# Performance work log

Hardware: AMD Instinct MI355X
Metric: run time of the kernel (lower is better)

## Reference

```python
import jax, jax.numpy as jnp
import numpy as np

N, K = 4096, 12          # nodes, incoming edges per node
E = N * K                # bonds
INPUT_DIM = 128
N_HEADS = 16
HEAD_DIM = 8
OUT_DIM = N_HEADS * HEAD_DIM   # 128
NUM_GAUSS = 20
NUM_ANG_FUNCS = 3              # AngularEncoding -> 1 + 3*2*2 = 13 dims
A_DIM = 1 + NUM_ANG_FUNCS * 4
KV_DIM = INPUT_DIM + 2 * NUM_GAUSS + A_DIM  # 181
Q_DIM = INPUT_DIM


def _build_graph_and_triplets():
    # edge e = i*K + t-1 : row=(i+t)%N -> col=i  (K incoming edges per node)
    col = np.repeat(np.arange(N), K)
    row = (col + np.tile(np.arange(1, K + 1), N)) % N
    bond_index = np.stack([row, col]).astype(np.int64)  # [2, E]
    # triplets: for edge e=(j->i), pair with every incoming edge (k->j) of j
    idx_ji = np.repeat(np.arange(E), K)
    idx_kj = np.repeat(row, K) * K + np.tile(np.arange(K), E)
    idx_i = col[idx_ji]
    idx_j = row[idx_ji]
    idx_k = row[idx_kj]
    mask = idx_i != idx_k
    return (bond_index, idx_i[mask], idx_j[mask], idx_k[mask],
            idx_kj[mask], idx_ji[mask])


def setup_inputs() -> dict:
    key = jax.random.key(0)
    ks = jax.random.split(key, 8)
    bond_index, idx_i, idx_j, idx_k, idx_kj, idx_ji = _build_graph_and_triplets()
    w = 0.05
    return {
        "h": jax.random.normal(ks[0], (N, INPUT_DIM), dtype=jnp.float32),
        "h_bond": jax.random.normal(ks[1], (E, INPUT_DIM), dtype=jnp.float32),
        "pos": jax.random.normal(ks[2], (N, 3), dtype=jnp.float32),
        "bond_index": jnp.asarray(bond_index),
        "idx_i": jnp.asarray(idx_i), "idx_j": jnp.asarray(idx_j),
        "idx_k": jnp.asarray(idx_k), "idx_kj": jnp.asarray(idx_kj),
        "idx_ji": jnp.asarray(idx_ji),
        "W_key": jax.random.normal(ks[3], (KV_DIM, OUT_DIM), dtype=jnp.float32) * w,
        "W_value": jax.random.normal(ks[4], (KV_DIM, OUT_DIM), dtype=jnp.float32) * w,
        "W_query": jax.random.normal(ks[5], (Q_DIM, OUT_DIM), dtype=jnp.float32) * w,
        "W_edge0": jax.random.normal(ks[6], (NUM_GAUSS, OUT_DIM), dtype=jnp.float32) * w,
        "W_edge1": jax.random.normal(ks[7], (NUM_GAUSS, OUT_DIM), dtype=jnp.float32) * w,
    }


def reference(h, h_bond, pos, bond_index, idx_i, idx_j, idx_k, idx_kj, idx_ji,
              W_key, W_value, W_query, W_edge0, W_edge1):
    Eb = h_bond.shape[0]
    row, col = bond_index[0], bond_index[1]
    # per-bond distance + Gaussian smearing (start=0, stop=10, 20 gaussians)
    dist = jnp.sqrt(jnp.sum((pos[col] - pos[row]) ** 2, axis=-1))  # [E]
    offset = jnp.linspace(0.0, 10.0, NUM_GAUSS)
    coeff = -0.5 / (offset[1] - offset[0]) ** 2
    r_feat = jnp.exp(coeff * (dist[:, None] - offset) ** 2)        # [E, 20]
    # per-triplet angle + angular encoding
    pos_i = pos[idx_i]
    pos_ji = pos[idx_j] - pos_i
    pos_ki = pos[idx_k] - pos_i
    a = jnp.sum(pos_ji * pos_ki, axis=-1)
    b = jnp.linalg.norm(jnp.cross(pos_ji, pos_ki), axis=-1)
    angle = jnp.arctan2(b, a)                                      # [T]
    t = jnp.arange(1, NUM_ANG_FUNCS + 1, dtype=jnp.float32)
    freq = jnp.concatenate([t, 1.0 / t])                           # [6]
    x = angle[:, None]
    a_feat = jnp.concatenate([x, jnp.sin(x * freq), jnp.cos(x * freq)], axis=-1)  # [T,13]
    # triplet gathers
    r_kj, r_ji = r_feat[idx_kj], r_feat[idx_ji]
    kv_input = jnp.concatenate([h_bond[idx_kj], r_kj, r_ji, a_feat], axis=-1)  # [T,181]
    q_input = h_bond[idx_ji]                                                    # [T,128]
    T = kv_input.shape[0]
    k_proj = (kv_input @ W_key).reshape(T, N_HEADS, HEAD_DIM)
    v_proj = (kv_input @ W_value).reshape(T, N_HEADS, HEAD_DIM)
    q_proj = (q_input @ W_query).reshape(T, N_HEADS, HEAD_DIM)
    edge_attn = jnp.tanh(r_ji @ W_edge0).reshape(T, N_HEADS, HEAD_DIM)
    alpha = jnp.sum(q_proj * k_proj * edge_attn, axis=-1) / np.sqrt(HEAD_DIM)   # [T,H]
    # segment softmax over idx_ji (torch_geometric softmax semantics)
    m = jax.lax.stop_gradient(jax.ops.segment_max(alpha, idx_ji, num_segments=Eb))
    ex = jnp.exp(alpha - m[idx_ji])
    s = jax.ops.segment_sum(ex, idx_ji, num_segments=Eb)
    alpha = ex / (s[idx_ji] + 1e-16)
    msg = v_proj * jnp.tanh(r_ji @ W_edge1).reshape(T, N_HEADS, HEAD_DIM)
    msg = msg * alpha[:, :, None]
    out = jax.ops.segment_sum(msg, idx_ji, num_segments=Eb)  # [E,H,D]
    return out.reshape(Eb, OUT_DIM)
```

## Files before the change

### kernel.cpp

```cpp
#include <hip/hip_runtime.h>
#include <math.h>

#define INPUT_DIM 128
#define OUT_DIM 128
#define NUM_GAUSS 20
#define NH 16
#define BM 64
#define MAXT 16
#define WPB 4
#define SCALE 0.35355339059327373f


static __device__ __forceinline__ void wave_lds_fence() {
    __asm__ volatile("s_waitcnt lgkmcnt(0)" ::: "memory");
    __builtin_amdgcn_wave_barrier();
}

__global__ __launch_bounds__(256, 3) void bond_proj_kernel(
    const float* __restrict__ h_bond,
    const float* __restrict__ pos,
    const int*   __restrict__ bond_index,
    const float* __restrict__ Wk,
    const float* __restrict__ Wv,
    const float* __restrict__ Wq,
    const float* __restrict__ We0,
    float* __restrict__ r_out,
    float* __restrict__ KB,
    float* __restrict__ VB,
    float* __restrict__ QE,
    int E)
{
    __shared__ float As[BM * 148];
    const int tid = threadIdx.x;
    const int e0 = blockIdx.x * BM;

    for (int i = tid; i < BM * 32; i += 256) {
        int e = i >> 5, c = (i & 31) << 2;
        float4 v = make_float4(0.f, 0.f, 0.f, 0.f);
        if (e0 + e < E) v = *(const float4*)&h_bond[(size_t)(e0 + e) * INPUT_DIM + c];
        float* dst = &As[e * 148 + c];
        dst[0] = v.x; dst[1] = v.y; dst[2] = v.z; dst[3] = v.w;
    }
    {
        const float step = 10.f / (NUM_GAUSS - 1);
        const float coeff = -0.5f / (step * step);
        for (int i = tid; i < BM * NUM_GAUSS; i += 256) {
            int e = i / NUM_GAUSS, g = i % NUM_GAUSS;
            int ge = e0 + e;
            float rv = 0.f;
            if (ge < E) {
                int jrow = bond_index[ge];
                int icol = bond_index[E + ge];
                float dx = pos[icol*3+0] - pos[jrow*3+0];
                float dy = pos[icol*3+1] - pos[jrow*3+1];
                float dz = pos[icol*3+2] - pos[jrow*3+2];
                float dist = sqrtf(dx*dx + dy*dy + dz*dz);
                float t = dist - g * step;
                rv = __expf(coeff * t * t);
                r_out[(size_t)ge * NUM_GAUSS + g] = rv;
            }
            As[e * 148 + 128 + g] = rv;
        }
    }
    __syncthreads();

    const int em = tid >> 5;
    const int dn = (tid & 31) << 2;
    const float* AsB = &As[em * 8 * 148];

    float aK[8][4], aV[8][4], aQ[8][4], aE[8][4];
    #pragma unroll
    for (int m = 0; m < 8; ++m)
        #pragma unroll
        for (int j = 0; j < 4; ++j) { aK[m][j]=0.f; aV[m][j]=0.f; aQ[m][j]=0.f; aE[m][j]=0.f; }

    #pragma unroll 2
    for (int c = 0; c < 128; ++c) {
        float4 wk = *(const float4*)&Wk[c * OUT_DIM + dn];
        float4 wv = *(const float4*)&Wv[c * OUT_DIM + dn];
        float4 wq = *(const float4*)&Wq[c * OUT_DIM + dn];
        #pragma unroll
        for (int m = 0; m < 8; ++m) {
            float a = AsB[m * 148 + c];
            aK[m][0] = fmaf(a, wk.x, aK[m][0]); aK[m][1] = fmaf(a, wk.y, aK[m][1]);
            aK[m][2] = fmaf(a, wk.z, aK[m][2]); aK[m][3] = fmaf(a, wk.w, aK[m][3]);
            aV[m][0] = fmaf(a, wv.x, aV[m][0]); aV[m][1] = fmaf(a, wv.y, aV[m][1]);
            aV[m][2] = fmaf(a, wv.z, aV[m][2]); aV[m][3] = fmaf(a, wv.w, aV[m][3]);
            aQ[m][0] = fmaf(a, wq.x, aQ[m][0]); aQ[m][1] = fmaf(a, wq.y, aQ[m][1]);
            aQ[m][2] = fmaf(a, wq.z, aQ[m][2]); aQ[m][3] = fmaf(a, wq.w, aQ[m][3]);
        }
    }
    #pragma unroll 2
    for (int g = 0; g < 20; ++g) {
        float4 wk = *(const float4*)&Wk[(INPUT_DIM + g) * OUT_DIM + dn];
        float4 wv = *(const float4*)&Wv[(INPUT_DIM + g) * OUT_DIM + dn];
        float4 w0 = *(const float4*)&We0[g * OUT_DIM + dn];
        #pragma unroll
        for (int m = 0; m < 8; ++m) {
            float a = AsB[m * 148 + 128 + g];
            aK[m][0] = fmaf(a, wk.x, aK[m][0]); aK[m][1] = fmaf(a, wk.y, aK[m][1]);
            aK[m][2] = fmaf(a, wk.z, aK[m][2]); aK[m][3] = fmaf(a, wk.w, aK[m][3]);
            aV[m][0] = fmaf(a, wv.x, aV[m][0]); aV[m][1] = fmaf(a, wv.y, aV[m][1]);
            aV[m][2] = fmaf(a, wv.z, aV[m][2]); aV[m][3] = fmaf(a, wv.w, aV[m][3]);
            aE[m][0] = fmaf(a, w0.x, aE[m][0]); aE[m][1] = fmaf(a, w0.y, aE[m][1]);
            aE[m][2] = fmaf(a, w0.z, aE[m][2]); aE[m][3] = fmaf(a, w0.w, aE[m][3]);
        }
    }

    #pragma unroll
    for (int m = 0; m < 8; ++m) {
        int e = e0 + em * 8 + m;
        if (e < E) {
            *(float4*)&KB[(size_t)e * OUT_DIM + dn] =
                make_float4(aK[m][0], aK[m][1], aK[m][2], aK[m][3]);
            *(float4*)&VB[(size_t)e * OUT_DIM + dn] =
                make_float4(aV[m][0], aV[m][1], aV[m][2], aV[m][3]);
            *(float4*)&QE[(size_t)e * OUT_DIM + dn] =
                make_float4(aQ[m][0] * tanhf(aE[m][0]), aQ[m][1] * tanhf(aE[m][1]),
                            aQ[m][2] * tanhf(aE[m][2]), aQ[m][3] * tanhf(aE[m][3]));
        }
    }
}

__global__ __launch_bounds__(256) void redge_kernel(
    const float* __restrict__ r_feat,
    const float* __restrict__ QE,
    const float* __restrict__ Wk,
    const float* __restrict__ Wv,
    const float* __restrict__ We1,
    float* __restrict__ EA1,
    float* __restrict__ ERV,
    float* __restrict__ QRK2,
    int E)
{
    __shared__ float Rs[BM][NUM_GAUSS];
    const int tid = threadIdx.x;
    const int e0 = blockIdx.x * BM;

    for (int i = tid; i < BM * 5; i += 256) {
        int e = i / 5, q = (i % 5) << 2;
        float4 v = make_float4(0.f, 0.f, 0.f, 0.f);
        if (e0 + e < E) v = *(const float4*)&r_feat[(size_t)(e0 + e) * NUM_GAUSS + q];
        Rs[e][q] = v.x; Rs[e][q+1] = v.y; Rs[e][q+2] = v.z; Rs[e][q+3] = v.w;
    }
    __syncthreads();

    const int em = tid >> 5;
    const int dn = (tid & 31) << 2;

    {
        float a1[8][4], aS[8][4];
        #pragma unroll
        for (int m = 0; m < 8; ++m)
            #pragma unroll
            for (int j = 0; j < 4; ++j) { a1[m][j] = 0.f; aS[m][j] = 0.f; }

        #pragma unroll 2
        for (int g = 0; g < 20; ++g) {
            float4 w1 = *(const float4*)&We1[g * OUT_DIM + dn];
            float4 wv = *(const float4*)&Wv[(148 + g) * OUT_DIM + dn];
            #pragma unroll
            for (int m = 0; m < 8; ++m) {
                float a = Rs[em * 8 + m][g];
                a1[m][0] = fmaf(a, w1.x, a1[m][0]); a1[m][1] = fmaf(a, w1.y, a1[m][1]);
                a1[m][2] = fmaf(a, w1.z, a1[m][2]); a1[m][3] = fmaf(a, w1.w, a1[m][3]);
                aS[m][0] = fmaf(a, wv.x, aS[m][0]); aS[m][1] = fmaf(a, wv.y, aS[m][1]);
                aS[m][2] = fmaf(a, wv.z, aS[m][2]); aS[m][3] = fmaf(a, wv.w, aS[m][3]);
            }
        }
        #pragma unroll
        for (int m = 0; m < 8; ++m) {
            int e = e0 + em * 8 + m;
            if (e < E) {
                float t0 = tanhf(a1[m][0]), t1 = tanhf(a1[m][1]);
                float t2 = tanhf(a1[m][2]), t3 = tanhf(a1[m][3]);
                *(float4*)&EA1[(size_t)e * OUT_DIM + dn] = make_float4(t0, t1, t2, t3);
                *(float4*)&ERV[(size_t)e * OUT_DIM + dn] =
                    make_float4(t0 * aS[m][0], t1 * aS[m][1], t2 * aS[m][2], t3 * aS[m][3]);
            }
        }
    }

    {
        float aR[8][4];
        #pragma unroll
        for (int m = 0; m < 8; ++m)
            #pragma unroll
            for (int j = 0; j < 4; ++j) aR[m][j] = 0.f;

        #pragma unroll 2
        for (int g = 0; g < 20; ++g) {
            float4 wk = *(const float4*)&Wk[(148 + g) * OUT_DIM + dn];
            #pragma unroll
            for (int m = 0; m < 8; ++m) {
                float a = Rs[em * 8 + m][g];
                aR[m][0] = fmaf(a, wk.x, aR[m][0]); aR[m][1] = fmaf(a, wk.y, aR[m][1]);
                aR[m][2] = fmaf(a, wk.z, aR[m][2]); aR[m][3] = fmaf(a, wk.w, aR[m][3]);
            }
        }
        const int hh = (tid & 31) >> 1;
        #pragma unroll
        for (int m = 0; m < 8; ++m) {
            int e = e0 + em * 8 + m;
            float s = 0.f;
            if (e < E) {
                float4 q = *(const float4*)&QE[(size_t)e * OUT_DIM + dn];
                s = q.x*aR[m][0] + q.y*aR[m][1] + q.z*aR[m][2] + q.w*aR[m][3];
            }
            s += __shfl_xor(s, 1);
            if ((tid & 1) == 0 && e < E) QRK2[(size_t)e * NH + hh] = s;
        }
    }
}

__global__ __launch_bounds__(256) void attn_wave_kernel(
    const float* __restrict__ pos,
    const int*   __restrict__ idx_i,
    const int*   __restrict__ idx_j,
    const int*   __restrict__ idx_k,
    const float* __restrict__ Wk,
    const float* __restrict__ Wv,
    const float* __restrict__ KB,
    const float* __restrict__ VB,
    const float* __restrict__ QE,
    const float* __restrict__ EA1,
    const float* __restrict__ ERV,
    const float* __restrict__ QRK2,
    float* __restrict__ out,
    int E)
{
    __shared__ float afL[WPB][2][12][13];

    unsigned bid = blockIdx.x, nwg = gridDim.x;
    unsigned qq = nwg >> 3, rr = nwg & 7, xc = bid & 7, rest = bid >> 3;
    unsigned swz = (xc < rr ? xc * (qq + 1) : rr * (qq + 1) + (xc - rr) * qq) + rest;

    const int l = threadIdx.x & 63;
    const int wvn = __builtin_amdgcn_readfirstlane(threadIdx.x >> 6);
    const int sg = l >> 5;
    const int s  = l & 31;
    const int e = (int)swz * (WPB * 2) + wvn * 2 + sg;
    if (e >= E) return;
    const int h = s >> 1;
    const int a = s & 1;
    const int d4 = 4 * s;

    const int ii = idx_i[(size_t)e * 12];
    const int jj = idx_j[(size_t)e * 12];
    const size_t kjb = (size_t)jj * 12;

    const float4 qe4  = *(const float4*)&QE [(size_t)e * OUT_DIM + d4];
    const float4 ea4  = *(const float4*)&EA1[(size_t)e * OUT_DIM + d4];
    const float4 erv4 = *(const float4*)&ERV[(size_t)e * OUT_DIM + d4];
    const float qrk2 = QRK2[(size_t)e * NH + h];

    const float pix = pos[ii*3+0], piy = pos[ii*3+1], piz = pos[ii*3+2];
    const float jx = pos[jj*3+0]-pix, jy = pos[jj*3+1]-piy, jz = pos[jj*3+2]-piz;
    if (s < 12) {
        int kk = idx_k[(size_t)e * 12 + s];
        float kx = pos[kk*3+0]-pix, ky = pos[kk*3+1]-piy, kz = pos[kk*3+2]-piz;
        float aa = jx*kx + jy*ky + jz*kz;
        float cx = jy*kz - jz*ky, cy = jz*kx - jx*kz, cz = jx*ky - jy*kx;
        float bb = sqrtf(cx*cx + cy*cy + cz*cz);
        float ang = atan2f(bb, aa);
        float af0[13];
        af0[0] = ang;
        const float fr[6] = {1.f, 2.f, 3.f, 1.f, 0.5f, 1.f/3.f};
        #pragma unroll
        for (int q = 0; q < 6; ++q)
            __sincosf(ang * fr[q], &af0[1+q], &af0[7+q]);
        #pragma unroll
        for (int c = 0; c < 13; ++c) afL[wvn][sg][s][c] = af0[c];
    }

    float qwk[13];
    #pragma unroll
    for (int c = 0; c < 13; ++c) {
        float4 w = *(const float4*)&Wk[(168 + c) * OUT_DIM + d4];
        float p = qe4.x*w.x + qe4.y*w.y + qe4.z*w.z + qe4.w*w.w;
        p += __shfl_xor(p, 1);
        qwk[c] = p;
    }

    float qk6[6];
    #pragma unroll
    for (int t = 0; t < 12; ++t) {
        float4 kb = *(const float4*)&KB[(kjb + t) * OUT_DIM + d4];
        float v = qe4.x*kb.x + qe4.y*kb.y + qe4.z*kb.z + qe4.w*kb.w;
        v += __shfl_xor(v, 1);
        if ((t & 1) == a) qk6[t >> 1] = v;
    }

    wave_lds_fence();

    float lg[6];
    #pragma unroll
    for (int q = 0; q < 6; ++q) {
        int t = 2*q + a;
        float ang = 0.f;
        #pragma unroll
        for (int c = 0; c < 13; ++c) ang = fmaf(afL[wvn][sg][t][c], qwk[c], ang);
        lg[q] = (qk6[q] + ang + qrk2) * SCALE;
    }

    float m = lg[0];
    #pragma unroll
    for (int q = 1; q < 6; ++q) m = fmaxf(m, lg[q]);
    m = fmaxf(m, __shfl_xor(m, 1));
    float ex[6], ss = 0.f;
    #pragma unroll
    for (int q = 0; q < 6; ++q) { ex[q] = __expf(lg[q] - m); ss += ex[q]; }
    ss += __shfl_xor(ss, 1);
    float inv = 1.f / (ss + 1e-16f);
    float al[6], alp[6];
    #pragma unroll
    for (int q = 0; q < 6; ++q) { al[q] = ex[q] * inv; alp[q] = __shfl_xor(al[q], 1); }
    float Sh = ss * inv;

    float waf[13];
    #pragma unroll
    for (int c = 0; c < 13; ++c) {
        float wp = 0.f;
        #pragma unroll
        for (int q = 0; q < 6; ++q) wp = fmaf(al[q], afL[wvn][sg][2*q + a][c], wp);
        wp += __shfl_xor(wp, 1);
        waf[c] = wp;
    }

    float ac0 = 0.f, ac1 = 0.f, ac2 = 0.f, ac3 = 0.f;
    #pragma unroll
    for (int t = 0; t < 12; ++t) {
        float4 vb = *(const float4*)&VB[(kjb + t) * OUT_DIM + d4];
        float at = ((t & 1) == a) ? al[t >> 1] : alp[t >> 1];
        ac0 = fmaf(at, vb.x, ac0); ac1 = fmaf(at, vb.y, ac1);
        ac2 = fmaf(at, vb.z, ac2); ac3 = fmaf(at, vb.w, ac3);
    }

    float vA0 = 0.f, vA1 = 0.f, vA2 = 0.f, vA3 = 0.f;
    #pragma unroll
    for (int c = 0; c < 13; ++c) {
        float4 w = *(const float4*)&Wv[(168 + c) * OUT_DIM + d4];
        vA0 = fmaf(waf[c], w.x, vA0); vA1 = fmaf(waf[c], w.y, vA1);
        vA2 = fmaf(waf[c], w.z, vA2); vA3 = fmaf(waf[c], w.w, vA3);
    }

    float4 o;
    o.x = ea4.x * (ac0 + vA0) + erv4.x * Sh;
    o.y = ea4.y * (ac1 + vA1) + erv4.y * Sh;
    o.z = ea4.z * (ac2 + vA2) + erv4.z * Sh;
    o.w = ea4.w * (ac3 + vA3) + erv4.w * Sh;
    *(float4*)&out[(size_t)e * OUT_DIM + d4] = o;
}

__global__ __launch_bounds__(128) void attn_generic_kernel(
    const float* __restrict__ pos,
    const int*   __restrict__ idx_i,
    const int*   __restrict__ idx_j,
    const int*   __restrict__ idx_k,
    const int*   __restrict__ idx_kj,
    const int*   __restrict__ idx_ji,
    const float* __restrict__ Wk,
    const float* __restrict__ Wv,
    const float* __restrict__ We1,
    const float* __restrict__ r_feat,
    const float* __restrict__ KB,
    const float* __restrict__ VB,
    const float* __restrict__ QE,
    float* __restrict__ out,
    int E, int T)
{
    __shared__ float rs[NUM_GAUSS];
    __shared__ float af[MAXT][13];
    __shared__ float logit[MAXT][NH];
    __shared__ float qwk[NH][13];
    __shared__ float waf[NH][13];
    __shared__ int   kjs[MAXT];
    __shared__ float qrk2s[NH];
    __shared__ float Shs[NH];

    const int e = blockIdx.x;
    const int d = threadIdx.x;
    const int h8 = d >> 3;

    int l = 0, hi = T;
    while (l < hi) { int mid = (l + hi) >> 1; if (idx_ji[mid] < e) l = mid + 1; else hi = mid; }
    int lo = l, c2 = 0;
    while (lo + c2 < T && c2 < MAXT && idx_ji[lo + c2] == e) ++c2;
    int cnt = c2;

    if (d < NUM_GAUSS) rs[d] = r_feat[(size_t)e * NUM_GAUSS + d];
    if (d < cnt) {
        int t = lo + d;
        kjs[d] = idx_kj[t];
        int ii = idx_i[t], jj = idx_j[t], kk = idx_k[t];
        float pix = pos[ii*3+0], piy = pos[ii*3+1], piz = pos[ii*3+2];
        float jx = pos[jj*3+0]-pix, jy = pos[jj*3+1]-piy, jz = pos[jj*3+2]-piz;
        float kx = pos[kk*3+0]-pix, ky = pos[kk*3+1]-piy, kz = pos[kk*3+2]-piz;
        float aa = jx*kx + jy*ky + jz*kz;
        float cx = jy*kz - jz*ky, cy = jz*kx - jx*kz, cz = jx*ky - jy*kx;
        float bb = sqrtf(cx*cx + cy*cy + cz*cz);
        float ang = atan2f(bb, aa);
        af[d][0] = ang;
        const float fr[6] = {1.f, 2.f, 3.f, 1.f, 0.5f, 1.f/3.f};
        #pragma unroll
        for (int q = 0; q < 6; ++q) {
            float s, cc;
            __sincosf(ang * fr[q], &s, &cc);
            af[d][1 + q] = s;
            af[d][7 + q] = cc;
        }
    }
    __syncthreads();

    const float qe = QE[(size_t)e * OUT_DIM + d];
    float s1 = 0.f, sk = 0.f, sv = 0.f;
    #pragma unroll
    for (int g = 0; g < NUM_GAUSS; ++g) {
        float rg = rs[g];
        s1 = fmaf(rg, We1[g * OUT_DIM + d], s1);
        sk = fmaf(rg, Wk[(148 + g) * OUT_DIM + d], sk);
        sv = fmaf(rg, Wv[(148 + g) * OUT_DIM + d], sv);
    }
    const float ea1 = tanhf(s1);
    const float rv2 = sv;

    {
        float v = qe * sk;
        v += __shfl_xor(v, 1, 8); v += __shfl_xor(v, 2, 8); v += __shfl_xor(v, 4, 8);
        if ((d & 7) == 0) qrk2s[h8] = v;
    }
    {
        float p[13];
        #pragma unroll
        for (int c = 0; c < 13; ++c) p[c] = qe * Wk[(168 + c) * OUT_DIM + d];
        #pragma unroll
        for (int c = 0; c < 13; ++c) {
            float v = p[c];
            v += __shfl_xor(v, 1, 8); v += __shfl_xor(v, 2, 8); v += __shfl_xor(v, 4, 8);
            if ((d & 7) == 0) qwk[h8][c] = v;
        }
    }
    for (int t = 0; t < cnt; ++t) {
        float lv = qe * KB[(size_t)kjs[t] * OUT_DIM + d];
        lv += __shfl_xor(lv, 1, 8); lv += __shfl_xor(lv, 2, 8); lv += __shfl_xor(lv, 4, 8);
        if ((d & 7) == 0) logit[t][h8] = lv;
    }
    __syncthreads();
    {
        const int hh = d & 15;
        for (int t = d >> 4; t < cnt; t += 8) {
            float s = 0.f;
            #pragma unroll
            for (int c = 0; c < 13; ++c) s = fmaf(af[t][c], qwk[hh][c], s);
            logit[t][hh] = (logit[t][hh] + s + qrk2s[hh]) * SCALE;
        }
    }
    __syncthreads();
    if (d < NH) {
        float m = -1e30f;
        for (int t = 0; t < cnt; ++t) m = fmaxf(m, logit[t][d]);
        float s = 0.f;
        for (int t = 0; t < cnt; ++t) { float ex = __expf(logit[t][d] - m); logit[t][d] = ex; s += ex; }
        float inv = 1.f / (s + 1e-16f);
        for (int t = 0; t < cnt; ++t) logit[t][d] *= inv;
        Shs[d] = s * inv;
    }
    __syncthreads();
    {
        const int hh = d & 15;
        int c = d >> 4;
        float w1 = 0.f;
        for (int t = 0; t < cnt; ++t) w1 = fmaf(logit[t][hh], af[t][c], w1);
        waf[hh][c] = w1;
        c += 8;
        if (c < 13) {
            float w2 = 0.f;
            for (int t = 0; t < cnt; ++t) w2 = fmaf(logit[t][hh], af[t][c], w2);
            waf[hh][c] = w2;
        }
    }
    __syncthreads();
    float vA = 0.f;
    #pragma unroll
    for (int c = 0; c < 13; ++c) vA = fmaf(waf[h8][c], Wv[(168 + c) * OUT_DIM + d], vA);
    float acc = 0.f;
    for (int t = 0; t < cnt; ++t)
        acc = fmaf(logit[t][h8], VB[(size_t)kjs[t] * OUT_DIM + d], acc);
    out[(size_t)e * OUT_DIM + d] = ea1 * (acc + vA + rv2 * Shs[h8]);
}

extern "C" void kernel_launch(void* const* d_in, const int* in_sizes, int n_in,
                              void* d_out, int out_size, void* d_ws, size_t ws_size,
                              hipStream_t stream) {
    const float* h_bond = (const float*)d_in[1];
    const float* pos    = (const float*)d_in[2];
    const int*   bidx   = (const int*)d_in[3];
    const int*   idx_i  = (const int*)d_in[4];
    const int*   idx_j  = (const int*)d_in[5];
    const int*   idx_k  = (const int*)d_in[6];
    const int*   idx_kj = (const int*)d_in[7];
    const int*   idx_ji = (const int*)d_in[8];
    const float* Wk     = (const float*)d_in[9];
    const float* Wv     = (const float*)d_in[10];
    const float* Wq     = (const float*)d_in[11];
    const float* We0    = (const float*)d_in[12];
    const float* We1    = (const float*)d_in[13];

    const int E = in_sizes[1] / INPUT_DIM;
    const int T = in_sizes[4];

    float* ws = (float*)d_ws;
    float* r_feat = ws;
    float* KB   = r_feat + (size_t)E * NUM_GAUSS;
    float* VB   = KB   + (size_t)E * OUT_DIM;
    float* QE   = VB   + (size_t)E * OUT_DIM;
    float* EA1  = QE   + (size_t)E * OUT_DIM;
    float* ERV  = EA1  + (size_t)E * OUT_DIM;
    float* QRK2 = ERV  + (size_t)E * OUT_DIM;

    bond_proj_kernel<<<(E + BM - 1) / BM, 256, 0, stream>>>(
        h_bond, pos, bidx, Wk, Wv, Wq, We0, r_feat, KB, VB, QE, E);

    redge_kernel<<<(E + BM - 1) / BM, 256, 0, stream>>>(
        r_feat, QE, Wk, Wv, We1, EA1, ERV, QRK2, E);

    if (T == E * 12) {
        const int segs_per_block = WPB * 2;
        attn_wave_kernel<<<(E + segs_per_block - 1) / segs_per_block, 64 * WPB, 0, stream>>>(
            pos, idx_i, idx_j, idx_k,
            Wk, Wv, KB, VB, QE, EA1, ERV, QRK2, (float*)d_out, E);
    } else {
        attn_generic_kernel<<<E, 128, 0, stream>>>(
            pos, idx_i, idx_j, idx_k, idx_kj, idx_ji,
            Wk, Wv, We1, r_feat, KB, VB, QE, (float*)d_out, E, T);
    }
}
```

Before: 162.2 us.

## Split bond projection across 1024-thread blocks with per-role warp groups

Blocks of bond_proj_kernel grow from 256 to 1024 threads. Threads 0-255 compute the K projection, 256-511 the V projection, and 512-1023 the Q and edge projections for half as many rows each. This replaces one thread holding 128 accumulators for four outputs with smaller per-thread register sets and more parallelism per tile. The cost is that each warp now reads the shared A tile separately, and the block size limits occupancy to one block per launch-bounds setting.

```diff
diff --git a/kernel.cpp b/kernel.cpp
--- a/kernel.cpp
+++ b/kernel.cpp
@@ -16,7 +16,7 @@
     __builtin_amdgcn_wave_barrier();
 }
 
-__global__ __launch_bounds__(256, 3) void bond_proj_kernel(
+__global__ __launch_bounds__(1024, 1) void bond_proj_kernel(
     const float* __restrict__ h_bond,
     const float* __restrict__ pos,
     const int*   __restrict__ bond_index,
@@ -34,7 +34,7 @@
     const int tid = threadIdx.x;
     const int e0 = blockIdx.x * BM;
 
-    for (int i = tid; i < BM * 32; i += 256) {
+    for (int i = tid; i < BM * 32; i += 1024) {
         int e = i >> 5, c = (i & 31) << 2;
         float4 v = make_float4(0.f, 0.f, 0.f, 0.f);
         if (e0 + e < E) v = *(const float4*)&h_bond[(size_t)(e0 + e) * INPUT_DIM + c];
@@ -44,7 +44,7 @@
     {
         const float step = 10.f / (NUM_GAUSS - 1);
         const float coeff = -0.5f / (step * step);
-        for (int i = tid; i < BM * NUM_GAUSS; i += 256) {
+        for (int i = tid; i < BM * NUM_GAUSS; i += 1024) {
             int e = i / NUM_GAUSS, g = i % NUM_GAUSS;
             int ge = e0 + e;
             float rv = 0.f;
@@ -64,60 +64,78 @@
     }
     __syncthreads();
 
-    const int em = tid >> 5;
-    const int dn = (tid & 31) << 2;
-    const float* AsB = &As[em * 8 * 148];
-
-    float aK[8][4], aV[8][4], aQ[8][4], aE[8][4];
-    #pragma unroll
-    for (int m = 0; m < 8; ++m)
-        #pragma unroll
-        for (int j = 0; j < 4; ++j) { aK[m][j]=0.f; aV[m][j]=0.f; aQ[m][j]=0.f; aE[m][j]=0.f; }
-
-    #pragma unroll 2
-    for (int c = 0; c < 128; ++c) {
-        float4 wk = *(const float4*)&Wk[c * OUT_DIM + dn];
-        float4 wv = *(const float4*)&Wv[c * OUT_DIM + dn];
-        float4 wq = *(const float4*)&Wq[c * OUT_DIM + dn];
+    const int role = tid >> 8;
+
+    if (role < 2) {
+        const float* __restrict__ W = (role == 0) ? Wk : Wv;
+        float* __restrict__ O = (role == 0) ? KB : VB;
+        const int t2 = tid & 255;
+        const int em = t2 >> 5;
+        const int dn = (t2 & 31) << 2;
+        const float* AsB = &As[em * 8 * 148];
+
+        float acc[8][4];
+        #pragma unroll
+        for (int m = 0; m < 8; ++m)
+            #pragma unroll
+            for (int j = 0; j < 4; ++j) acc[m][j] = 0.f;
+
+        #pragma unroll 2
+        for (int c = 0; c < 148; ++c) {
+            float4 w = *(const float4*)&W[c * OUT_DIM + dn];
+            #pragma unroll
+            for (int m = 0; m < 8; ++m) {
+                float a = AsB[m * 148 + c];
+                acc[m][0] = fmaf(a, w.x, acc[m][0]); acc[m][1] = fmaf(a, w.y, acc[m][1]);
+                acc[m][2] = fmaf(a, w.z, acc[m][2]); acc[m][3] = fmaf(a, w.w, acc[m][3]);
+            }
+        }
         #pragma unroll
         for (int m = 0; m < 8; ++m) {
-            float a = AsB[m * 148 + c];
-            aK[m][0] = fmaf(a, wk.x, aK[m][0]); aK[m][1] = fmaf(a, wk.y, aK[m][1]);
-            aK[m][2] = fmaf(a, wk.z, aK[m][2]); aK[m][3] = fmaf(a, wk.w, aK[m][3]);
-            aV[m][0] = fmaf(a, wv.x, aV[m][0]); aV[m][1] = fmaf(a, wv.y, aV[m][1]);
-            aV[m][2] = fmaf(a, wv.z, aV[m][2]); aV[m][3] = fmaf(a, wv.w, aV[m][3]);
-            aQ[m][0] = fmaf(a, wq.x, aQ[m][0]); aQ[m][1] = fmaf(a, wq.y, aQ[m][1]);
-            aQ[m][2] = fmaf(a, wq.z, aQ[m][2]); aQ[m][3] = fmaf(a, wq.w, aQ[m][3]);
-        }
-    }
-    #pragma unroll 2
-    for (int g = 0; g < 20; ++g) {
-        float4 wk = *(const float4*)&Wk[(INPUT_DIM + g) * OUT_DIM + dn];
-        float4 wv = *(const float4*)&Wv[(INPUT_DIM + g) * OUT_DIM + dn];
-        float4 w0 = *(const float4*)&We0[g * OUT_DIM + dn];
-        #pragma unroll
-        for (int m = 0; m < 8; ++m) {
-            float a = AsB[m * 148 + 128 + g];
-            aK[m][0] = fmaf(a, wk.x, aK[m][0]); aK[m][1] = fmaf(a, wk.y, aK[m][1]);
-            aK[m][2] = fmaf(a, wk.z, aK[m][2]); aK[m][3] = fmaf(a, wk.w, aK[m][3]);
-            aV[m][0] = fmaf(a, wv.x, aV[m][0]); aV[m][1] = fmaf(a, wv.y, aV[m][1]);
-            aV[m][2] = fmaf(a, wv.z, aV[m][2]); aV[m][3] = fmaf(a, wv.w, aV[m][3]);
-            aE[m][0] = fmaf(a, w0.x, aE[m][0]); aE[m][1] = fmaf(a, w0.y, aE[m][1]);
-            aE[m][2] = fmaf(a, w0.z, aE[m][2]); aE[m][3] = fmaf(a, w0.w, aE[m][3]);
-        }
-    }
-
-    #pragma unroll
-    for (int m = 0; m < 8; ++m) {
-        int e = e0 + em * 8 + m;
-        if (e < E) {
-            *(float4*)&KB[(size_t)e * OUT_DIM + dn] =
-                make_float4(aK[m][0], aK[m][1], aK[m][2], aK[m][3]);
-            *(float4*)&VB[(size_t)e * OUT_DIM + dn] =
-                make_float4(aV[m][0], aV[m][1], aV[m][2], aV[m][3]);
-            *(float4*)&QE[(size_t)e * OUT_DIM + dn] =
-                make_float4(aQ[m][0] * tanhf(aE[m][0]), aQ[m][1] * tanhf(aE[m][1]),
-                            aQ[m][2] * tanhf(aE[m][2]), aQ[m][3] * tanhf(aE[m][3]));
+            int e = e0 + em * 8 + m;
+            if (e < E)
+                *(float4*)&O[(size_t)e * OUT_DIM + dn] =
+                    make_float4(acc[m][0], acc[m][1], acc[m][2], acc[m][3]);
+        }
+    } else {
+        const int t2 = tid & 511;
+        const int em = t2 >> 5;
+        const int dn = (t2 & 31) << 2;
+        const float* AsB = &As[em * 4 * 148];
+
+        float aQ[4][4], aE[4][4];
+        #pragma unroll
+        for (int m = 0; m < 4; ++m)
+            #pragma unroll
+            for (int j = 0; j < 4; ++j) { aQ[m][j] = 0.f; aE[m][j] = 0.f; }
+
+        #pragma unroll 2
+        for (int c = 0; c < 128; ++c) {
+            float4 wq = *(const float4*)&Wq[c * OUT_DIM + dn];
+            #pragma unroll
+            for (int m = 0; m < 4; ++m) {
+                float a = AsB[m * 148 + c];
+                aQ[m][0] = fmaf(a, wq.x, aQ[m][0]); aQ[m][1] = fmaf(a, wq.y, aQ[m][1]);
+                aQ[m][2] = fmaf(a, wq.z, aQ[m][2]); aQ[m][3] = fmaf(a, wq.w, aQ[m][3]);
+            }
+        }
+        #pragma unroll 2
+        for (int g = 0; g < 20; ++g) {
+            float4 w0 = *(const float4*)&We0[g * OUT_DIM + dn];
+            #pragma unroll
+            for (int m = 0; m < 4; ++m) {
+                float a = AsB[m * 148 + 128 + g];
+                aE[m][0] = fmaf(a, w0.x, aE[m][0]); aE[m][1] = fmaf(a, w0.y, aE[m][1]);
+                aE[m][2] = fmaf(a, w0.z, aE[m][2]); aE[m][3] = fmaf(a, w0.w, aE[m][3]);
+            }
+        }
+        #pragma unroll
+        for (int m = 0; m < 4; ++m) {
+            int e = e0 + em * 4 + m;
+            if (e < E)
+                *(float4*)&QE[(size_t)e * OUT_DIM + dn] =
+                    make_float4(aQ[m][0] * tanhf(aE[m][0]), aQ[m][1] * tanhf(aE[m][1]),
+                                aQ[m][2] * tanhf(aE[m][2]), aQ[m][3] * tanhf(aE[m][3]));
         }
     }
 }
@@ -518,7 +536,7 @@
     float* ERV  = EA1  + (size_t)E * OUT_DIM;
     float* QRK2 = ERV  + (size_t)E * OUT_DIM;
 
-    bond_proj_kernel<<<(E + BM - 1) / BM, 256, 0, stream>>>(
+    bond_proj_kernel<<<(E + BM - 1) / BM, 1024, 0, stream>>>(
         h_bond, pos, bidx, Wk, Wv, Wq, We0, r_feat, KB, VB, QE, E);
 
     redge_kernel<<<(E + BM - 1) / BM, 256, 0, stream>>>(
```

Result: no change. 162.0 us (-0.1%).
